# Performance work log

Measured on AMD Instinct MI355X. Metric: run time of the kernel, lower is better.

## Reference

```python
import jax, jax.numpy as jnp
import numpy as np
from jax import lax

# Normalized separable resample filter [1,3,3,1] (upfirdn2d.setup_filter divides by sum)
_F1 = np.array([1.0, 3.0, 3.0, 1.0]); _F1 /= _F1.sum()
_F2D = np.outer(_F1, _F1)  # 4x4, sums to 1
_CLAMP = 256.0
_LRELU_GAIN = np.sqrt(2.0)  # def_gain of lrelu in bias_act


def _depthwise(x, f2d):
    C = x.shape[1]
    k = jnp.broadcast_to(f2d[None, None], (C, 1, f2d.shape[0], f2d.shape[1])).astype(x.dtype)
    return lax.conv_general_dilated(x, k, (1, 1), [(0, 0), (0, 0)],
                                    dimension_numbers=('NCHW', 'OIHW', 'NCHW'),
                                    feature_group_count=C)


def _upfirdn_up2(x, pad, gain):
    # zero-insert upsample by 2, pad, FIR filter with given gain (upfirdn2d reference)
    B, C, H, W = x.shape
    x = jnp.pad(x.reshape(B, C, H, 1, W, 1), ((0, 0), (0, 0), (0, 0), (0, 1), (0, 0), (0, 1)))
    x = x.reshape(B, C, 2 * H, 2 * W)
    py0, py1, px0, px1 = pad
    x = jnp.pad(x, ((0, 0), (0, 0), (py0, py1), (px0, px1)))
    return _depthwise(x, jnp.asarray(_F2D * gain, x.dtype))


def _conv(x, w, pad):
    return lax.conv_general_dilated(x, w, (1, 1), [(pad, pad), (pad, pad)],
                                    dimension_numbers=('NCHW', 'OIHW', 'NCHW'))


def _mod_conv(x, weight, styles, demodulate, up, padding):
    # modulated_conv2d: modulate input by styles, shared-weight conv, demod output.
    # Mathematically identical to the fused grouped-conv path.
    if demodulate:
        w = weight[None] * styles[:, None, :, None, None]           # [B,Cout,Cin,kh,kw]
        dcoefs = lax.rsqrt(jnp.sum(w * w, axis=(2, 3, 4)) + 1e-8)   # [B,Cout]
    x = x * styles[:, :, None, None]
    if up == 2:
        # conv2d_resample(up=2): upfirdn2d(up=2, pad=(padding+2, padding+1), gain=4)
        # then conv with flipped weight (flip_weight=False)
        x = _upfirdn_up2(x, (padding + 2, padding + 1, padding + 2, padding + 1), 4.0)
        x = _conv(x, weight[:, :, ::-1, ::-1], 0)
    else:
        x = _conv(x, weight, padding)
    if demodulate:
        x = x * dcoefs[:, :, None, None]
    return x


def _bias_lrelu_clamp(x, b):
    x = x + b[None, :, None, None]
    x = jnp.where(x >= 0, x, 0.2 * x) * _LRELU_GAIN
    return jnp.clip(x, -_CLAMP, _CLAMP)


def setup_inputs() -> dict:
    key = jax.random.key(0)
    ks = jax.random.split(key, 16)
    B, CIN, COUT, WD, RES, IMG_CH = 8, 512, 512, 512, 64, 3
    return {
        'x': jax.random.normal(ks[0], (B, CIN, RES // 2, RES // 2), jnp.float32),
        'img': jax.random.normal(ks[1], (B, IMG_CH, RES // 2, RES // 2), jnp.float32),
        'ws': jax.random.normal(ks[2], (B, 3, WD), jnp.float32),
        'affine0_w': jax.random.normal(ks[3], (CIN, WD), jnp.float32),
        'affine0_b': jnp.ones((CIN,), jnp.float32),
        'weight0': jax.random.normal(ks[4], (COUT, CIN, 3, 3), jnp.float32),
        'bias0': jnp.zeros((COUT,), jnp.float32),
        'noise_strength0': jax.random.normal(ks[5], (1,), jnp.float32),
        'noise_const0': jax.random.normal(ks[6], (RES, RES), jnp.float32),
        'affine1_w': jax.random.normal(ks[7], (COUT, WD), jnp.float32),
        'affine1_b': jnp.ones((COUT,), jnp.float32),
        'weight1': jax.random.normal(ks[8], (COUT, COUT, 3, 3), jnp.float32),
        'bias1': jnp.zeros((COUT,), jnp.float32),
        'noise_strength1': jax.random.normal(ks[9], (1,), jnp.float32),
        'noise_const1': jax.random.normal(ks[10], (RES, RES), jnp.float32),
        'affine_rgb_w': jax.random.normal(ks[11], (COUT, WD), jnp.float32),
        'affine_rgb_b': jnp.ones((COUT,), jnp.float32),
        'weight_rgb': jax.random.normal(ks[12], (IMG_CH, COUT, 1, 1), jnp.float32),
        'bias_rgb': jnp.zeros((IMG_CH,), jnp.float32),
    }


def reference(x, img, ws, affine0_w, affine0_b, weight0, bias0, noise_strength0, noise_const0,
              affine1_w, affine1_b, weight1, bias1, noise_strength1, noise_const1,
              affine_rgb_w, affine_rgb_b, weight_rgb, bias_rgb):
    sg = 1.0 / np.sqrt(ws.shape[-1])  # FullyConnectedLayer weight_gain
    # conv0: up=2, demodulated, const noise, lrelu+clamp
    s0 = ws[:, 0] @ affine0_w.T * sg + affine0_b
    x = _mod_conv(x, weight0, s0, True, 2, 1)
    x = x + noise_const0[None, None] * noise_strength0[0]
    x = _bias_lrelu_clamp(x, bias0)
    # conv1: up=1
    s1 = ws[:, 1] @ affine1_w.T * sg + affine1_b
    x = _mod_conv(x, weight1, s1, True, 1, 1)
    x = x + noise_const1[None, None] * noise_strength1[0]
    x = _bias_lrelu_clamp(x, bias1)
    # skip: upsample img (upsample2d: pad=(2,1), gain=4)
    img = _upfirdn_up2(img, (2, 1, 2, 1), 4.0)
    # torgb: 1x1 modulated conv, no demod, styles scaled by 1/sqrt(Cin)
    srgb = (ws[:, 2] @ affine_rgb_w.T * sg + affine_rgb_b) * (1.0 / np.sqrt(weight_rgb.shape[1]))
    y = _mod_conv(x, weight_rgb, srgb, False, 1, 0)
    y = jnp.clip(y + bias_rgb[None, :, None, None], -_CLAMP, _CLAMP)
    img = img + y
    return (x, img)
```

## Files before the change

kernel.cpp:

```cpp
#include <hip/hip_runtime.h>
#include <hip/hip_bf16.h>
#include <stdint.h>

#define DEV __device__ __forceinline__

typedef float f32x4 __attribute__((ext_vector_type(4)));
typedef short s16x8 __attribute__((ext_vector_type(8)));
typedef __bf16 bf16x8 __attribute__((ext_vector_type(8)));
typedef unsigned short us8 __attribute__((ext_vector_type(8)));
typedef unsigned short u16;

DEV u16 f2bf(float f) {
  uint32_t u = __builtin_bit_cast(uint32_t, f);
  u += 0x7FFFu + ((u >> 16) & 1u);
  return (u16)(u >> 16);
}
DEV float bf2f(u16 h) { return __builtin_bit_cast(float, (uint32_t)h << 16); }

DEV void gload16(const void* g, void* l) {
  __builtin_amdgcn_global_load_lds((__attribute__((address_space(1))) void*)(g),
                                   (__attribute__((address_space(3))) void*)(l),
                                   16, 0, 0);
}

DEV f32x4 mfma16(s16x8 a, s16x8 b, f32x4 c) {
  return __builtin_amdgcn_mfma_f32_16x16x32_bf16(
      __builtin_bit_cast(bf16x8, a), __builtin_bit_cast(bf16x8, b), c, 0, 0, 0);
}

#define OFF_S0    0ul
#define OFF_S1    16384ul
#define OFF_SRGB  32768ul
#define OFF_D0    49152ul
#define OFF_D1    65536ul
#define OFF_WSQ0  81920ul
#define OFF_WSQ1  1130496ul
#define OFF_ZERO  2179072ul
#define OFF_X0M   2179328ul
#define OFF_W0T   10567936ul
#define OFF_W1T   15286528ul
#define OFF_ZZ    20005120ul
#define OFF_X1M   55689472ul

__global__ void styles_kernel(const float* __restrict__ wsv,
                              const float* __restrict__ a0w, const float* __restrict__ a0b,
                              const float* __restrict__ a1w, const float* __restrict__ a1b,
                              const float* __restrict__ argw, const float* __restrict__ argb,
                              float* __restrict__ s0, float* __restrict__ s1,
                              float* __restrict__ srgb) {
  const int idx = blockIdx.x * 4 + (threadIdx.x >> 6);
  const int lane = threadIdx.x & 63;
  const int l = idx >> 12, rem = idx & 4095, b = rem >> 9, o = rem & 511;
  const float* aw = (l == 0) ? a0w : ((l == 1) ? a1w : argw);
  const float* wrow = wsv + (b * 3 + l) * 512;
  const float* arow = aw + o * 512;
  float acc = 0.f;
#pragma unroll
  for (int k = 0; k < 8; ++k) acc += wrow[lane + 64 * k] * arow[lane + 64 * k];
#pragma unroll
  for (int off = 32; off; off >>= 1) acc += __shfl_xor(acc, off);
  if (lane == 0) {
    const float sg = 0.04419417382415922f;
    if (l == 0)      s0[b * 512 + o] = acc * sg + a0b[o];
    else if (l == 1) s1[b * 512 + o] = acc * sg + a1b[o];
    else             srgb[b * 512 + o] = (acc * sg + argb[o]) * sg;
  }
}

__global__ void prepWT_kernel(const float* __restrict__ w, u16* __restrict__ wt,
                              float* __restrict__ wsq) {
  const int idx = blockIdx.x * 256 + threadIdx.x;
  float v[9], sq = 0.f;
#pragma unroll
  for (int t = 0; t < 9; ++t) { v[t] = w[idx * 9 + t]; sq += v[t] * v[t]; }
  wsq[idx] = sq;
#pragma unroll
  for (int t = 0; t < 9; ++t) wt[(size_t)t * 262144 + idx] = f2bf(v[t]);
}

__global__ void dcoef_kernel(const float* __restrict__ s0, const float* __restrict__ s1,
                             const float* __restrict__ wsq0, const float* __restrict__ wsq1,
                             float* __restrict__ d0, float* __restrict__ d1) {
  const int idx = blockIdx.x * 4 + (threadIdx.x >> 6);
  const int lane = threadIdx.x & 63;
  const int layer = idx >> 12, rem = idx & 4095, b = rem >> 9, o = rem & 511;
  const float* s = layer ? s1 : s0;
  const float* wsq = layer ? wsq1 : wsq0;
  float acc = 0.f;
#pragma unroll
  for (int k = 0; k < 8; ++k) {
    const int c = lane + 64 * k;
    const float sv = s[b * 512 + c];
    acc += sv * sv * wsq[o * 512 + c];
  }
#pragma unroll
  for (int off = 32; off; off >>= 1) acc += __shfl_xor(acc, off);
  if (lane == 0) (layer ? d1 : d0)[b * 512 + o] = 1.f / sqrtf(acc + 1e-8f);
}

__global__ void x0m_kernel(const float* __restrict__ x, const float* __restrict__ s0,
                           u16* __restrict__ out) {
  __shared__ u16 t[32 * 514];
  const int b = blockIdx.x >> 5, h = blockIdx.x & 31;
  const int tid = threadIdx.x;
  const int w = tid & 31, cs = tid >> 5;
  for (int c0 = 0; c0 < 512; c0 += 8) {
    const int c = c0 + cs;
    t[w * 514 + c] = f2bf(x[((b * 512 + c) * 32 + h) * 32 + w] * s0[b * 512 + c]);
  }
  __syncthreads();
  const int base = ((b * 32 + h) * 32) * 512;
  for (int i = 0; i < 64; ++i) {
    const int idx = i * 256 + tid;
    out[base + idx] = t[(idx >> 9) * 514 + (idx & 511)];
  }
}

template <int PH>
DEV void phaseconv_body(char* smem, int tid, int lane, int wid, int l15, int l4,
                        int obase, int tile, int b,
                        const char* xin_c, const char* wt_c, u16* __restrict__ zz,
                        const char* __restrict__ zerobuf) {
  constexpr int NT = (PH == 0) ? 4 : ((PH == 3) ? 1 : 2);
  constexpr int SLt[4][4] = {{8, 6, 2, 0}, {7, 1, 0, 0}, {5, 3, 0, 0}, {4, 0, 0, 0}};
  constexpr int TYt[4][4] = {{0, 0, 1, 1}, {0, 1, 0, 0}, {1, 1, 0, 0}, {1, 0, 0, 0}};
  constexpr int TXt[4][4] = {{0, 1, 0, 1}, {1, 1, 0, 0}, {0, 1, 0, 0}, {1, 0, 0, 0}};
  constexpr int A_OFF = 24576;

  const int p0 = tile * 256;
  const int r0 = (p0 * 993) >> 15;
  const int row0 = r0 - 1;

  size_t boff[6];
  bool bval[6];
#pragma unroll
  for (int i = 0; i < 6; ++i) {
    const int u = i * 256 + tid;
    const int row = u / 136;
    const int rem = u - row * 136;
    const int k8 = rem / 34;
    const int col = rem - k8 * 34;
    const int ir = row0 + row;
    const int ic = col - 1;
    bval[i] = (u < 1360) && (ir >= 0) && (ir < 32) && (ic >= 0) && (ic < 32);
    boff[i] = ((size_t)((b * 32 + ir) * 32 + ic) * 512 + k8 * 8) * 2;
  }

  int ub[4], pp[4];
#pragma unroll
  for (int bc = 0; bc < 4; ++bc) {
    const int p = p0 + wid * 64 + bc * 16 + l15;
    pp[bc] = p;
    const int qy = (p * 993) >> 15;
    const int qx = p - qy * 33;
    ub[bc] = (((qy - r0) * 4 + l4) * 34 + qx) * 16;
  }

  const size_t aoffb = ((size_t)(obase + lane) * 512 + (size_t)wid * 8) * 2;

  f32x4 acc[4][4];
  const f32x4 fz = {0.f, 0.f, 0.f, 0.f};
#pragma unroll
  for (int i = 0; i < 4; ++i)
#pragma unroll
    for (int j = 0; j < 4; ++j) acc[i][j] = fz;

  for (int c0 = 0; c0 < 512; c0 += 32) {
#pragma unroll
    for (int i = 0; i < 6; ++i) {
      const void* src = bval[i] ? (const void*)(xin_c + boff[i] + (size_t)c0 * 2)
                                : (const void*)zerobuf;
      gload16(src, smem + i * 4096 + wid * 1024);
    }
#pragma unroll
    for (int t = 0; t < NT; ++t)
      gload16(wt_c + (size_t)SLt[PH][t] * 524288 + aoffb + (size_t)c0 * 2,
              smem + A_OFF + t * 4096 + wid * 1024);
    __syncthreads();
#pragma unroll
    for (int t = 0; t < NT; ++t) {
      s16x8 bfr[4], afr[4];
#pragma unroll
      for (int bc = 0; bc < 4; ++bc)
        bfr[bc] = *(const s16x8*)(smem + ub[bc] + (TYt[PH][t] * 136 + TXt[PH][t]) * 16);
#pragma unroll
      for (int f = 0; f < 4; ++f)
        afr[f] = *(const s16x8*)(smem + A_OFF + t * 4096 + (l4 * 64 + f * 16 + l15) * 16);
#pragma unroll
      for (int f = 0; f < 4; ++f)
#pragma unroll
        for (int bc = 0; bc < 4; ++bc)
          acc[f][bc] = mfma16(afr[f], bfr[bc], acc[f][bc]);
    }
    __syncthreads();
  }

#pragma unroll
  for (int f = 0; f < 4; ++f) {
    const int o = obase + f * 16 + l4 * 4;
#pragma unroll
    for (int bc = 0; bc < 4; ++bc) {
      if (pp[bc] < 1089) {
        ushort4 pk;
        pk.x = f2bf(acc[f][bc][0]);
        pk.y = f2bf(acc[f][bc][1]);
        pk.z = f2bf(acc[f][bc][2]);
        pk.w = f2bf(acc[f][bc][3]);
        *(ushort4*)(zz + ((size_t)(PH * 8 + b) * 1089 + pp[bc]) * 512 + o) = pk;
      }
    }
  }
}

__global__ __launch_bounds__(256, 3) void phaseconv_kernel(
    const u16* __restrict__ xin, const u16* __restrict__ wt, u16* __restrict__ zz,
    const char* __restrict__ zerobuf) {
  __shared__ __align__(16) char smem[40960];
  const int tid = threadIdx.x;
  const int lane = tid & 63, wid = tid >> 6, l15 = lane & 15, l4 = lane >> 4;
  const int bid = blockIdx.x;
  const int ph = bid / 320;
  const int rr = bid - ph * 320;
  const int obIdx = rr & 7;
  const int r = rr >> 3;
  const int tile = r % 5;
  const int b = r / 5;
  const int obase = obIdx * 64;
  const char* xin_c = (const char*)xin;
  const char* wt_c = (const char*)wt;
  switch (ph) {
    case 0: phaseconv_body<0>(smem, tid, lane, wid, l15, l4, obase, tile, b, xin_c, wt_c, zz, zerobuf); break;
    case 1: phaseconv_body<1>(smem, tid, lane, wid, l15, l4, obase, tile, b, xin_c, wt_c, zz, zerobuf); break;
    case 2: phaseconv_body<2>(smem, tid, lane, wid, l15, l4, obase, tile, b, xin_c, wt_c, zz, zerobuf); break;
    default: phaseconv_body<3>(smem, tid, lane, wid, l15, l4, obase, tile, b, xin_c, wt_c, zz, zerobuf); break;
  }
}

__global__ __launch_bounds__(256) void fir_kernel(
    const u16* __restrict__ zz, const float* __restrict__ dc0,
    const float* __restrict__ bias0, const float* __restrict__ noise0,
    const float* __restrict__ ns0, const float* __restrict__ s1,
    u16* __restrict__ x1m) {
  const int u = blockIdx.x & 63, b = blockIdx.x >> 6;
  const int tid = threadIdx.x;
  const int lane = tid & 63, vg = tid >> 6;
  const int c = lane * 8;
  const float kk[4] = {0.25f, 0.75f, 0.75f, 0.25f};

  float wy[4]; int ry[4], qy[4];
#pragma unroll
  for (int k = 0; k < 4; ++k) {
    const int my = u - 1 + k;
    wy[k] = (my >= 0) ? kk[k] : 0.f;
    ry[k] = my & 1;
    qy[k] = (my >= 0) ? (my >> 1) : 0;
  }
  float dcv[8], bv[8], sv[8];
#pragma unroll
  for (int r = 0; r < 8; ++r) {
    dcv[r] = dc0[b * 512 + c + r];
    bv[r]  = bias0[c + r];
    sv[r]  = s1[b * 512 + c + r];
  }
  const float nsc = ns0[0];

  for (int vi = 0; vi < 16; ++vi) {
    const int v = vg * 16 + vi;
    float wx[4]; int rx[4], qx[4];
#pragma unroll
    for (int k = 0; k < 4; ++k) {
      const int mx = v - 1 + k;
      wx[k] = (mx >= 0) ? kk[k] : 0.f;
      rx[k] = mx & 1;
      qx[k] = (mx >= 0) ? (mx >> 1) : 0;
    }
    float a[8] = {0.f, 0.f, 0.f, 0.f, 0.f, 0.f, 0.f, 0.f};
#pragma unroll
    for (int ky = 0; ky < 4; ++ky)
#pragma unroll
      for (int kx = 0; kx < 4; ++kx) {
        const size_t off = ((size_t)((ry[ky] * 2 + rx[kx]) * 8 + b) * 1089 +
                            qy[ky] * 33 + qx[kx]) * 512 + c;
        const us8 zv = *(const us8*)(zz + off);
        const float w = wy[ky] * wx[kx];
#pragma unroll
        for (int r = 0; r < 8; ++r) a[r] = fmaf(w, bf2f(zv[r]), a[r]);
      }
    const float nz = noise0[u * 64 + v] * nsc;
    us8 pk;
#pragma unroll
    for (int r = 0; r < 8; ++r) {
      float xv = a[r] * dcv[r] + nz + bv[r];
      xv = (xv < 0.f ? 0.2f * xv : xv) * 1.4142135623730951f;
      xv = fminf(fmaxf(xv, -256.f), 256.f);
      pk[r] = f2bf(xv * sv[r]);
    }
    *(us8*)(x1m + ((size_t)((b * 64 + u) * 64 + v) * 512 + c)) = pk;
  }
}

__global__ __launch_bounds__(256, 2) void conv1_kernel(
    const u16* __restrict__ xin, const u16* __restrict__ wt,
    const float* __restrict__ dcoef, const float* __restrict__ bias,
    const float* __restrict__ noise, const float* __restrict__ nstr,
    float* __restrict__ out_f32, const char* __restrict__ zerobuf) {
  __shared__ __align__(16) char smem[65536];
  const int tid = threadIdx.x;
  const int lane = tid & 63, wid = tid >> 6, l15 = lane & 15, l4 = lane >> 4;

  int bid = blockIdx.x;
  const int obIdx = bid & 7; bid >>= 3;
  const int tile = bid & 15;
  const int b = bid >> 4;
  const int obase = obIdx * 64;
  const int row0 = tile * 4 - 1;

  size_t boff[7];
  bool bval[7];
#pragma unroll
  for (int i = 0; i < 7; ++i) {
    const int u = i * 256 + tid;
    const int row = u / 264;
    const int rem = u - row * 264;
    const int k8 = rem / 66;
    const int col = rem - k8 * 66;
    const int ir = row0 + row;
    const int ic = col - 1;
    bval[i] = (row < 6) && (ir >= 0) && (ir < 64) && (ic >= 0) && (ic < 64);
    boff[i] = ((size_t)((b * 64 + ir) * 64 + ic) * 512 + k8 * 8) * 2;
  }

  int ub[4], jy[4], jx[4];
#pragma unroll
  for (int bc = 0; bc < 4; ++bc) {
    const int p = wid * 64 + bc * 16 + l15;
    const int pr = p >> 6, pc = p & 63;
    ub[bc] = ((pr * 4 + l4) * 66 + pc) * 16;
    jy[bc] = tile * 4 + pr;
    jx[bc] = pc;
  }

  const char* wt_c = (const char*)wt;
  const char* xin_c = (const char*)xin;
  const size_t aoffb = ((size_t)(obase + lane) * 512 + (size_t)wid * 8) * 2;

  f32x4 acc[4][4];
  const f32x4 fz = {0.f, 0.f, 0.f, 0.f};
#pragma unroll
  for (int i = 0; i < 4; ++i)
#pragma unroll
    for (int j = 0; j < 4; ++j) acc[i][j] = fz;

  for (int c0 = 0; c0 < 512; c0 += 32) {
#pragma unroll
    for (int i = 0; i < 7; ++i) {
      const void* src = bval[i] ? (const void*)(xin_c + boff[i] + (size_t)c0 * 2)
                                : (const void*)zerobuf;
      gload16(src, smem + i * 4096 + wid * 1024);
    }
#pragma unroll
    for (int t = 0; t < 9; ++t)
      gload16(wt_c + (size_t)t * 524288 + aoffb + (size_t)c0 * 2,
              smem + 28672 + t * 4096 + wid * 1024);
    __syncthreads();
#pragma unroll
    for (int t = 0; t < 9; ++t) {
      const int dyi = t / 3, dxi = t % 3;
      s16x8 bfr[4], afr[4];
#pragma unroll
      for (int bc = 0; bc < 4; ++bc)
        bfr[bc] = *(const s16x8*)(smem + ub[bc] + (dyi * 264 + dxi) * 16);
#pragma unroll
      for (int f = 0; f < 4; ++f)
        afr[f] = *(const s16x8*)(smem + 28672 + t * 4096 + (l4 * 64 + f * 16 + l15) * 16);
#pragma unroll
      for (int f = 0; f < 4; ++f)
#pragma unroll
        for (int bc = 0; bc < 4; ++bc)
          acc[f][bc] = mfma16(afr[f], bfr[bc], acc[f][bc]);
    }
    __syncthreads();
  }

  const float ns = nstr[0];
#pragma unroll
  for (int f = 0; f < 4; ++f) {
    const int o = obase + f * 16 + l4 * 4;
    const f32x4 dc = *(const f32x4*)(dcoef + b * 512 + o);
    const f32x4 bs = *(const f32x4*)(bias + o);
#pragma unroll
    for (int bc = 0; bc < 4; ++bc) {
      const float nz = noise[jy[bc] * 64 + jx[bc]] * ns;
#pragma unroll
      for (int r = 0; r < 4; ++r) {
        float xv = acc[f][bc][r] * dc[r] + nz + bs[r];
        xv = (xv < 0.f ? 0.2f * xv : xv) * 1.4142135623730951f;
        xv = fminf(fmaxf(xv, -256.f), 256.f);
        out_f32[((size_t)(b * 512 + o + r) * 64 + jy[bc]) * 64 + jx[bc]] = xv;
      }
    }
  }
}

__global__ void torgb_kernel(const float* __restrict__ xw, const float* __restrict__ img,
                             const float* __restrict__ srgb, const float* __restrict__ wrgb,
                             const float* __restrict__ brgb, float* __restrict__ imgout) {
  __shared__ float red[4][3][64];
  const int b = blockIdx.x >> 6, jy = blockIdx.x & 63;
  const int tid = threadIdx.x;
  const int jx = tid & 63, cg = tid >> 6;
  float p0 = 0.f, p1 = 0.f, p2 = 0.f;
  const float* xb = xw + ((size_t)(b * 512 + cg * 128) * 64 + jy) * 64 + jx;
  const float* sb = srgb + b * 512 + cg * 128;
  for (int i = 0; i < 128; ++i) {
    const float xs = xb[(size_t)i * 4096] * sb[i];
    const int c = cg * 128 + i;
    p0 += xs * wrgb[c];
    p1 += xs * wrgb[512 + c];
    p2 += xs * wrgb[1024 + c];
  }
  red[cg][0][jx] = p0; red[cg][1][jx] = p1; red[cg][2][jx] = p2;
  __syncthreads();
  if (cg == 0) {
    const int qy = jy >> 1, qx = jx >> 1;
    int ry[2]; float wy[2];
    if ((jy & 1) == 0) { ry[0] = qy - 1; wy[0] = 0.25f; ry[1] = qy; wy[1] = 0.75f; }
    else               { ry[0] = qy;     wy[0] = 0.75f; ry[1] = qy + 1; wy[1] = 0.25f; }
    int rx[2]; float wx[2];
    if ((jx & 1) == 0) { rx[0] = qx - 1; wx[0] = 0.25f; rx[1] = qx; wx[1] = 0.75f; }
    else               { rx[0] = qx;     wx[0] = 0.75f; rx[1] = qx + 1; wx[1] = 0.25f; }
#pragma unroll
    for (int o = 0; o < 3; ++o) {
      float y = red[0][o][jx] + red[1][o][jx] + red[2][o][jx] + red[3][o][jx] + brgb[o];
      y = fminf(fmaxf(y, -256.f), 256.f);
      float iv = 0.f;
#pragma unroll
      for (int a = 0; a < 2; ++a)
#pragma unroll
        for (int e = 0; e < 2; ++e)
          if (ry[a] >= 0 && ry[a] < 32 && rx[e] >= 0 && rx[e] < 32)
            iv += wy[a] * wx[e] * img[((b * 3 + o) * 32 + ry[a]) * 32 + rx[e]];
      imgout[((b * 3 + o) * 64 + jy) * 64 + jx] = y + iv;
    }
  }
}

extern "C" void kernel_launch(void* const* d_in, const int* in_sizes, int n_in,
                              void* d_out, int out_size, void* d_ws, size_t ws_size,
                              hipStream_t stream) {
  (void)in_sizes; (void)n_in; (void)out_size; (void)ws_size;
  const float* x    = (const float*)d_in[0];
  const float* img  = (const float*)d_in[1];
  const float* wsv  = (const float*)d_in[2];
  const float* a0w  = (const float*)d_in[3];
  const float* a0b  = (const float*)d_in[4];
  const float* w0   = (const float*)d_in[5];
  const float* b0   = (const float*)d_in[6];
  const float* ns0  = (const float*)d_in[7];
  const float* nc0  = (const float*)d_in[8];
  const float* a1w  = (const float*)d_in[9];
  const float* a1b  = (const float*)d_in[10];
  const float* w1   = (const float*)d_in[11];
  const float* b1   = (const float*)d_in[12];
  const float* ns1  = (const float*)d_in[13];
  const float* nc1  = (const float*)d_in[14];
  const float* argw = (const float*)d_in[15];
  const float* argb = (const float*)d_in[16];
  const float* wrgb = (const float*)d_in[17];
  const float* brgb = (const float*)d_in[18];

  char* wsb = (char*)d_ws;
  float* s0   = (float*)(wsb + OFF_S0);
  float* s1   = (float*)(wsb + OFF_S1);
  float* srgb = (float*)(wsb + OFF_SRGB);
  float* dd0  = (float*)(wsb + OFF_D0);
  float* dd1  = (float*)(wsb + OFF_D1);
  float* wsq0 = (float*)(wsb + OFF_WSQ0);
  float* wsq1 = (float*)(wsb + OFF_WSQ1);
  char*  zero = wsb + OFF_ZERO;
  u16*   x0m  = (u16*)(wsb + OFF_X0M);
  u16*   w0t  = (u16*)(wsb + OFF_W0T);
  u16*   w1t  = (u16*)(wsb + OFF_W1T);
  u16*   zz   = (u16*)(wsb + OFF_ZZ);
  u16*   x1m  = (u16*)(wsb + OFF_X1M);

  float* out_x   = (float*)d_out;
  float* out_img = out_x + 16777216;

  hipMemsetAsync(zero, 0, 256, stream);
  styles_kernel<<<3072, 256, 0, stream>>>(wsv, a0w, a0b, a1w, a1b, argw, argb, s0, s1, srgb);
  prepWT_kernel<<<1024, 256, 0, stream>>>(w0, w0t, wsq0);
  prepWT_kernel<<<1024, 256, 0, stream>>>(w1, w1t, wsq1);
  dcoef_kernel<<<2048, 256, 0, stream>>>(s0, s1, wsq0, wsq1, dd0, dd1);
  x0m_kernel<<<256, 256, 0, stream>>>(x, s0, x0m);
  phaseconv_kernel<<<1280, 256, 0, stream>>>(x0m, w0t, zz, zero);
  fir_kernel<<<512, 256, 0, stream>>>(zz, dd0, b0, nc0, ns0, s1, x1m);
  conv1_kernel<<<1024, 256, 0, stream>>>(x1m, w1t, dd1, b1, nc1, ns1, out_x, zero);
  torgb_kernel<<<512, 256, 0, stream>>>(out_x, img, srgb, wrgb, brgb, out_img);
}
```

Baseline: 459.4 us.

## Widen phase-conv blocks to share input tile and stage FIR through LDS

```diff
diff --git a/kernel.cpp b/kernel.cpp
--- a/kernel.cpp
+++ b/kernel.cpp
@@ -117,8 +117,8 @@
 }
 
 template <int PH>
-DEV void phaseconv_body(char* smem, int tid, int lane, int wid, int l15, int l4,
-                        int obase, int tile, int b,
+DEV void phaseconv_body(char* smem, int tid, int lane, int wid,
+                        int obp, int tile, int b,
                         const char* xin_c, const char* wt_c, u16* __restrict__ zz,
                         const char* __restrict__ zerobuf) {
   constexpr int NT = (PH == 0) ? 4 : ((PH == 3) ? 1 : 2);
@@ -127,15 +127,20 @@
   constexpr int TXt[4][4] = {{0, 1, 0, 1}, {1, 1, 0, 0}, {0, 1, 0, 0}, {1, 0, 0, 0}};
   constexpr int A_OFF = 24576;
 
+  const int l15 = lane & 15, l4 = lane >> 4;
+  const int cg = wid >> 2;
+  const int pg = wid & 3;
+  const int obase = obp * 128 + cg * 64;
+
   const int p0 = tile * 256;
   const int r0 = (p0 * 993) >> 15;
   const int row0 = r0 - 1;
 
-  size_t boff[6];
-  bool bval[6];
-#pragma unroll
-  for (int i = 0; i < 6; ++i) {
-    const int u = i * 256 + tid;
+  size_t boff[3];
+  bool bval[3];
+#pragma unroll
+  for (int i = 0; i < 3; ++i) {
+    const int u = i * 512 + tid;
     const int row = u / 136;
     const int rem = u - row * 136;
     const int k8 = rem / 34;
@@ -149,14 +154,14 @@
   int ub[4], pp[4];
 #pragma unroll
   for (int bc = 0; bc < 4; ++bc) {
-    const int p = p0 + wid * 64 + bc * 16 + l15;
+    const int p = p0 + pg * 64 + bc * 16 + l15;
     pp[bc] = p;
     const int qy = (p * 993) >> 15;
     const int qx = p - qy * 33;
     ub[bc] = (((qy - r0) * 4 + l4) * 34 + qx) * 16;
   }
 
-  const size_t aoffb = ((size_t)(obase + lane) * 512 + (size_t)wid * 8) * 2;
+  const size_t aoffb = ((size_t)(obp * 128 + (tid & 127)) * 512 + (size_t)(tid >> 7) * 8) * 2;
 
   f32x4 acc[4][4];
   const f32x4 fz = {0.f, 0.f, 0.f, 0.f};
@@ -167,15 +172,15 @@
 
   for (int c0 = 0; c0 < 512; c0 += 32) {
 #pragma unroll
-    for (int i = 0; i < 6; ++i) {
+    for (int i = 0; i < 3; ++i) {
       const void* src = bval[i] ? (const void*)(xin_c + boff[i] + (size_t)c0 * 2)
                                 : (const void*)zerobuf;
-      gload16(src, smem + i * 4096 + wid * 1024);
+      gload16(src, smem + i * 8192 + wid * 1024);
     }
 #pragma unroll
     for (int t = 0; t < NT; ++t)
       gload16(wt_c + (size_t)SLt[PH][t] * 524288 + aoffb + (size_t)c0 * 2,
-              smem + A_OFF + t * 4096 + wid * 1024);
+              smem + A_OFF + t * 8192 + wid * 1024);
     __syncthreads();
 #pragma unroll
     for (int t = 0; t < NT; ++t) {
@@ -185,7 +190,8 @@
         bfr[bc] = *(const s16x8*)(smem + ub[bc] + (TYt[PH][t] * 136 + TXt[PH][t]) * 16);
 #pragma unroll
       for (int f = 0; f < 4; ++f)
-        afr[f] = *(const s16x8*)(smem + A_OFF + t * 4096 + (l4 * 64 + f * 16 + l15) * 16);
+        afr[f] = *(const s16x8*)(smem + A_OFF + t * 8192 +
+                                 (l4 * 128 + cg * 64 + f * 16 + l15) * 16);
 #pragma unroll
       for (int f = 0; f < 4; ++f)
 #pragma unroll
@@ -212,27 +218,26 @@
   }
 }
 
-__global__ __launch_bounds__(256, 3) void phaseconv_kernel(
+__global__ __launch_bounds__(512, 2) void phaseconv_kernel(
     const u16* __restrict__ xin, const u16* __restrict__ wt, u16* __restrict__ zz,
     const char* __restrict__ zerobuf) {
-  __shared__ __align__(16) char smem[40960];
+  __shared__ __align__(16) char smem[57344];
   const int tid = threadIdx.x;
-  const int lane = tid & 63, wid = tid >> 6, l15 = lane & 15, l4 = lane >> 4;
+  const int lane = tid & 63, wid = tid >> 6;
   const int bid = blockIdx.x;
-  const int ph = bid / 320;
-  const int rr = bid - ph * 320;
-  const int obIdx = rr & 7;
-  const int r = rr >> 3;
-  const int tile = r % 5;
-  const int b = r / 5;
-  const int obase = obIdx * 64;
+  const int ph = bid / 160;
+  const int rem = bid - ph * 160;
+  const int tile = rem >> 5;
+  const int rem2 = rem & 31;
+  const int b = rem2 >> 2;
+  const int obp = rem2 & 3;
   const char* xin_c = (const char*)xin;
   const char* wt_c = (const char*)wt;
   switch (ph) {
-    case 0: phaseconv_body<0>(smem, tid, lane, wid, l15, l4, obase, tile, b, xin_c, wt_c, zz, zerobuf); break;
-    case 1: phaseconv_body<1>(smem, tid, lane, wid, l15, l4, obase, tile, b, xin_c, wt_c, zz, zerobuf); break;
-    case 2: phaseconv_body<2>(smem, tid, lane, wid, l15, l4, obase, tile, b, xin_c, wt_c, zz, zerobuf); break;
-    default: phaseconv_body<3>(smem, tid, lane, wid, l15, l4, obase, tile, b, xin_c, wt_c, zz, zerobuf); break;
+    case 0: phaseconv_body<0>(smem, tid, lane, wid, obp, tile, b, xin_c, wt_c, zz, zerobuf); break;
+    case 1: phaseconv_body<1>(smem, tid, lane, wid, obp, tile, b, xin_c, wt_c, zz, zerobuf); break;
+    case 2: phaseconv_body<2>(smem, tid, lane, wid, obp, tile, b, xin_c, wt_c, zz, zerobuf); break;
+    default: phaseconv_body<3>(smem, tid, lane, wid, obp, tile, b, xin_c, wt_c, zz, zerobuf); break;
   }
 }
 
@@ -241,61 +246,82 @@
     const float* __restrict__ bias0, const float* __restrict__ noise0,
     const float* __restrict__ ns0, const float* __restrict__ s1,
     u16* __restrict__ x1m) {
-  const int u = blockIdx.x & 63, b = blockIdx.x >> 6;
+  __shared__ __align__(16) char smem[65280];
   const int tid = threadIdx.x;
-  const int lane = tid & 63, vg = tid >> 6;
-  const int c = lane * 8;
+  const int cg = blockIdx.x & 15;
+  const int t  = (blockIdx.x >> 4) & 7;
+  const int b  = blockIdx.x >> 7;
+  const int c0 = cg * 32;
+
+  const us8 zv0 = {0, 0, 0, 0, 0, 0, 0, 0};
+  for (int it = 0; it < 13; ++it) {
+    const int u = it * 256 + tid;
+    if (u < 3264) {
+      const int cell = u >> 2, j = u & 3;
+      const int ry = cell / 408;
+      const int r1 = cell - ry * 408;
+      const int qyi = r1 / 68;
+      const int r2 = r1 - qyi * 68;
+      const int rx = r2 / 34;
+      const int qxi = r2 - rx * 34;
+      const int qy = 4 * t - 1 + qyi;
+      const int qx = qxi - 1;
+      us8 v = zv0;
+      if (qy >= 0 && qy <= 32 && qx >= 0 && qx <= 32)
+        v = *(const us8*)(zz + ((size_t)((ry * 2 + rx) * 8 + b) * 1089 + qy * 33 + qx) * 512 +
+                          c0 + j * 8);
+      *(us8*)(smem + cell * 80 + j * 16) = v;
+    }
+  }
+  __syncthreads();
+
+  const int v = tid & 63, cs = tid >> 6;
+  const int cc = c0 + cs * 8;
   const float kk[4] = {0.25f, 0.75f, 0.75f, 0.25f};
-
-  float wy[4]; int ry[4], qy[4];
-#pragma unroll
-  for (int k = 0; k < 4; ++k) {
-    const int my = u - 1 + k;
-    wy[k] = (my >= 0) ? kk[k] : 0.f;
-    ry[k] = my & 1;
-    qy[k] = (my >= 0) ? (my >> 1) : 0;
-  }
+  const int rx0 = (v - 1) & 1, qxi0 = ((v - 1) >> 1) + 1;
+  const int rx1 = v & 1,       qxi1 = (v >> 1) + 1;
+  const int ho0 = rx0 * 34 * 80 + qxi0 * 80 + cs * 16;
+  const int ho1 = rx1 * 34 * 80 + qxi1 * 80 + cs * 16;
+
+  float tmp[11][8];
+#pragma unroll
+  for (int i = 0; i < 11; ++i) {
+    const int ry = (i + 1) & 1, qyi = (i + 1) >> 1;
+    const char* pb = smem + ((ry * 6 + qyi) * 2) * 34 * 80;
+    const us8 a0 = *(const us8*)(pb + ho0);
+    const us8 a2 = *(const us8*)(pb + ho0 + 80);
+    const us8 a1 = *(const us8*)(pb + ho1);
+    const us8 a3 = *(const us8*)(pb + ho1 + 80);
+#pragma unroll
+    for (int r = 0; r < 8; ++r)
+      tmp[i][r] = kk[0] * bf2f(a0[r]) + kk[2] * bf2f(a2[r]) +
+                  kk[1] * bf2f(a1[r]) + kk[3] * bf2f(a3[r]);
+  }
+
   float dcv[8], bv[8], sv[8];
 #pragma unroll
   for (int r = 0; r < 8; ++r) {
-    dcv[r] = dc0[b * 512 + c + r];
-    bv[r]  = bias0[c + r];
-    sv[r]  = s1[b * 512 + c + r];
+    dcv[r] = dc0[b * 512 + cc + r];
+    bv[r]  = bias0[cc + r];
+    sv[r]  = s1[b * 512 + cc + r];
   }
   const float nsc = ns0[0];
 
-  for (int vi = 0; vi < 16; ++vi) {
-    const int v = vg * 16 + vi;
-    float wx[4]; int rx[4], qx[4];
-#pragma unroll
-    for (int k = 0; k < 4; ++k) {
-      const int mx = v - 1 + k;
-      wx[k] = (mx >= 0) ? kk[k] : 0.f;
-      rx[k] = mx & 1;
-      qx[k] = (mx >= 0) ? (mx >> 1) : 0;
-    }
-    float a[8] = {0.f, 0.f, 0.f, 0.f, 0.f, 0.f, 0.f, 0.f};
-#pragma unroll
-    for (int ky = 0; ky < 4; ++ky)
-#pragma unroll
-      for (int kx = 0; kx < 4; ++kx) {
-        const size_t off = ((size_t)((ry[ky] * 2 + rx[kx]) * 8 + b) * 1089 +
-                            qy[ky] * 33 + qx[kx]) * 512 + c;
-        const us8 zv = *(const us8*)(zz + off);
-        const float w = wy[ky] * wx[kx];
-#pragma unroll
-        for (int r = 0; r < 8; ++r) a[r] = fmaf(w, bf2f(zv[r]), a[r]);
-      }
+#pragma unroll
+  for (int ui = 0; ui < 8; ++ui) {
+    const int u = 8 * t + ui;
     const float nz = noise0[u * 64 + v] * nsc;
     us8 pk;
 #pragma unroll
     for (int r = 0; r < 8; ++r) {
-      float xv = a[r] * dcv[r] + nz + bv[r];
+      float a = kk[0] * tmp[ui][r] + kk[1] * tmp[ui + 1][r] +
+                kk[2] * tmp[ui + 2][r] + kk[3] * tmp[ui + 3][r];
+      float xv = a * dcv[r] + nz + bv[r];
       xv = (xv < 0.f ? 0.2f * xv : xv) * 1.4142135623730951f;
       xv = fminf(fmaxf(xv, -256.f), 256.f);
       pk[r] = f2bf(xv * sv[r]);
     }
-    *(us8*)(x1m + ((size_t)((b * 64 + u) * 64 + v) * 512 + c)) = pk;
+    *(us8*)(x1m + ((size_t)((b * 64 + u) * 64 + v) * 512 + cc)) = pk;
   }
 }
 
@@ -493,8 +519,8 @@
   prepWT_kernel<<<1024, 256, 0, stream>>>(w1, w1t, wsq1);
   dcoef_kernel<<<2048, 256, 0, stream>>>(s0, s1, wsq0, wsq1, dd0, dd1);
   x0m_kernel<<<256, 256, 0, stream>>>(x, s0, x0m);
-  phaseconv_kernel<<<1280, 256, 0, stream>>>(x0m, w0t, zz, zero);
-  fir_kernel<<<512, 256, 0, stream>>>(zz, dd0, b0, nc0, ns0, s1, x1m);
+  phaseconv_kernel<<<640, 512, 0, stream>>>(x0m, w0t, zz, zero);
+  fir_kernel<<<1024, 256, 0, stream>>>(zz, dd0, b0, nc0, ns0, s1, x1m);
   conv1_kernel<<<1024, 256, 0, stream>>>(x1m, w1t, dd1, b1, nc1, ns1, out_x, zero);
   torgb_kernel<<<512, 256, 0, stream>>>(out_x, img, srgb, wrgb, brgb, out_img);
 }
```

Measured after the change: 448.0 us. 2.5% less time.
